# Kernel tuning notes

Hardware: AMD Instinct MI355X
Metric: run time of the kernel (lower is better)

The kernel has to match this reference:

```python
import jax, jax.numpy as jnp
import numpy as np

E = 50000      # entity_total
R = 100        # relation_total
DIM = 128      # config.dim
M = 10         # max_context_num
M1 = M + 1
T = 2 * R + 2  # entity_gcn_weight rows (2R+1) + appended zero row
B = 1024


def setup_inputs() -> dict:
    key = jax.random.key(0)
    ks = jax.random.split(key, 40)
    f = jnp.float32
    stdv = 1.0 / np.sqrt(DIM)
    inp = {}
    inp['entity_emb'] = jax.random.normal(ks[0], (E, DIM), f) * 0.05
    inp['relation_emb'] = jax.random.normal(ks[1], (R, DIM), f) * 0.05
    ec = jax.random.normal(ks[2], (E + 1, DIM), f) * 0.05
    inp['entity_context'] = ec.at[E].set(0.0)   # padding_idx row = 0
    rc = jax.random.normal(ks[3], (R + 1, DIM), f) * 0.05
    inp['relation_context'] = rc.at[R].set(0.0)
    inp['entity_gcn_weight'] = jax.random.uniform(ks[4], (2 * R + 1, DIM, DIM), f, -stdv, stdv)
    inp['relation_gcn_weight'] = jax.random.uniform(ks[5], (DIM, DIM), f, -stdv, stdv)
    inp['gate_entity'] = jax.random.uniform(ks[6], (DIM,), f)
    inp['gate_relation'] = jax.random.uniform(ks[7], (DIM,), f)
    inp['v_ent'] = jax.random.uniform(ks[8], (DIM,), f)
    inp['v_rel'] = jax.random.uniform(ks[9], (DIM,), f)
    inp['pos_h'] = jax.random.randint(ks[10], (B,), 0, E)
    inp['pos_r'] = jax.random.randint(ks[11], (B,), 0, R)
    inp['pos_t'] = jax.random.randint(ks[12], (B,), 0, E)
    inp['neg_h'] = jax.random.randint(ks[13], (B,), 0, E)
    inp['neg_r'] = jax.random.randint(ks[14], (B,), 0, R)
    inp['neg_t'] = jax.random.randint(ks[15], (B,), 0, E)
    inp['ph_adj'] = jax.random.randint(ks[16], (B, M), 0, E + 1)
    inp['pt_adj'] = jax.random.randint(ks[17], (B, M), 0, E + 1)
    inp['nh_adj'] = jax.random.randint(ks[18], (B, M), 0, E + 1)
    inp['nt_adj'] = jax.random.randint(ks[19], (B, M), 0, E + 1)
    inp['pr_adj'] = jax.random.randint(ks[20], (B, M, 2), 0, R + 1)
    inp['nr_adj'] = jax.random.randint(ks[21], (B, M, 2), 0, R + 1)
    inp['ph_R'] = jax.random.randint(ks[22], (B, M1, M1), 0, T)
    inp['pt_R'] = jax.random.randint(ks[23], (B, M1, M1), 0, T)
    inp['nh_R'] = jax.random.randint(ks[24], (B, M1, M1), 0, T)
    inp['nt_R'] = jax.random.randint(ks[25], (B, M1, M1), 0, T)
    inp['ph_nn'] = jax.random.randint(ks[26], (B,), 0, M)
    inp['pt_nn'] = jax.random.randint(ks[27], (B,), 0, M)
    inp['nh_nn'] = jax.random.randint(ks[28], (B,), 0, M)
    inp['nt_nn'] = jax.random.randint(ks[29], (B,), 0, M)
    inp['ph_D'] = jax.random.uniform(ks[30], (B, M1, M1), f)
    inp['pt_D'] = jax.random.uniform(ks[31], (B, M1, M1), f)
    inp['nh_D'] = jax.random.uniform(ks[32], (B, M1, M1), f)
    inp['nt_D'] = jax.random.uniform(ks[33], (B, M1, M1), f)
    inp['pr_A'] = jax.random.normal(ks[34], (B, M1, M1), f)
    inp['nr_A'] = jax.random.normal(ks[35], (B, M1, M1), f)
    return inp


def reference(entity_emb, relation_emb, entity_context, relation_context,
              entity_gcn_weight, relation_gcn_weight, gate_entity, gate_relation,
              v_ent, v_rel,
              pos_h, pos_r, pos_t, neg_h, neg_r, neg_t,
              ph_adj, pt_adj, nh_adj, nt_adj, pr_adj, nr_adj,
              ph_R, pt_R, nh_R, nt_R, ph_nn, pt_nn, nh_nn, nt_nn,
              ph_D, pt_D, nh_D, nt_D, pr_A, nr_A):
    # weight table with trailing zero row (padding relation type T-1)
    Wfull = jnp.concatenate(
        [entity_gcn_weight, jnp.zeros((1, DIM, DIM), entity_gcn_weight.dtype)], axis=0)

    def ent_ctx(vec, adj_idx):
        # center vector + M gathered context vectors -> [B, M1, d]
        return jnp.concatenate([vec[:, None, :], entity_context[adj_idx]], axis=1)

    def rel_ctx(vec, adj_idx):
        # relation context comes in (head,tail) pairs, summed over the 2
        a = relation_context[adj_idx].sum(axis=2)  # [B, M, d]
        return jnp.concatenate([vec[:, None, :], a], axis=1)

    def rgcn(Rt, Dm, nn_, H):
        # vectorized R-GCN: out[b,j] = relu(sum_k D[b,j,k] * H[b,j] @ W[Rt[b,j,k]])
        # restricted to the dynamic (n+1)x(n+1) block via masking.
        j = jnp.arange(M1)
        valid = j[None, :] <= nn_[:, None]                 # [B, M1]
        pair = valid[:, :, None] & valid[:, None, :]       # [B, M1, M1]
        Rm = jnp.where(pair, Rt, T - 1)                    # pad -> zero weight
        Dd = jnp.where(pair, Dm, jnp.zeros((), Dm.dtype))
        # segment-reduce D over relation types: C[b,j,t] = sum_{k: Rm=t} D[b,j,k]
        C = (jax.nn.one_hot(Rm, T, dtype=H.dtype) * Dd[..., None]).sum(axis=2)  # [B,M1,T]
        S = jnp.einsum('bjt,tde->bjde', C, Wfull)          # [B, M1, d, d]
        out = jax.nn.relu(jnp.einsum('bjd,bjde->bje', H, S))
        return jnp.where(valid[..., None], out, jnp.zeros((), out.dtype))

    def gcn_rel(A, H):
        return jax.nn.relu(jnp.einsum('bij,bjd,de->bie', A, H, relation_gcn_weight))

    def subgraph(o, adj, v):
        # attention over context rows, then weighted sum
        tmp = jax.nn.relu(adj * o[:, None, :])             # [B, M1, d]
        alpha = jax.nn.softmax(tmp @ v, axis=1)            # [B, M1]
        return jnp.sum(alpha[..., None] * adj, axis=1)     # [B, d]

    p_h = entity_emb[pos_h]; p_t = entity_emb[pos_t]; p_r = relation_emb[pos_r]
    n_h = entity_emb[neg_h]; n_t = entity_emb[neg_t]; n_r = relation_emb[neg_r]

    ph_v = rgcn(ph_R, ph_D, ph_nn, ent_ctx(p_h, ph_adj))
    pt_v = rgcn(pt_R, pt_D, pt_nn, ent_ctx(p_t, pt_adj))
    nh_v = rgcn(nh_R, nh_D, nh_nn, ent_ctx(n_h, nh_adj))
    nt_v = rgcn(nt_R, nt_D, nt_nn, ent_ctx(n_t, nt_adj))
    pr_v = gcn_rel(pr_A, rel_ctx(p_r, pr_adj))
    nr_v = gcn_rel(nr_A, rel_ctx(n_r, nr_adj))

    ph_sg = subgraph(p_h, ph_v, v_ent); pt_sg = subgraph(p_t, pt_v, v_ent)
    nh_sg = subgraph(n_h, nh_v, v_ent); nt_sg = subgraph(n_t, nt_v, v_ent)
    pr_sg = subgraph(p_r, pr_v, v_rel); nr_sg = subgraph(n_r, nr_v, v_rel)

    ge = jax.nn.sigmoid(gate_entity)
    gr = jax.nn.sigmoid(gate_relation)
    ph_o = ge * p_h + (1 - ge) * ph_sg
    pt_o = ge * p_t + (1 - ge) * pt_sg
    nh_o = ge * n_h + (1 - ge) * nh_sg
    nt_o = ge * n_t + (1 - ge) * nt_sg
    pr_o = gr * p_r + (1 - gr) * pr_sg
    nr_o = gr * n_r + (1 - gr) * nr_sg

    p_score = jnp.linalg.norm(ph_o + pr_o - pt_o, ord=2, axis=1)
    n_score = jnp.linalg.norm(nh_o + nr_o - nt_o, ord=2, axis=1)
    return (p_score, n_score)
```

## Files before the change

### kernel.cpp

```cpp
#include <hip/hip_runtime.h>
#include <math.h>

#define B_   1024
#define M_   10
#define M1_  11
#define DIM_ 128
#define NW_  201
#define NQUAD_ (4*B_*M1_*M1_)
#define IPB_  64
#define SLOTS_ 2048
#define NSPLIT_ 16
#define SCATB_ 121
#define WTILES_ ((NW_+1)*16)

typedef __attribute__((ext_vector_type(8))) short bf16x8;
typedef __attribute__((ext_vector_type(4))) float f32x4;

struct GatherPtrs {
    const int* center[4];
    const int* adj[4];
    const int* nn[4];
    const int* Rt[4];
    const float* Dm[4];
};

struct RelPtrs {
    const int* center[2];
    const int* adj2[2];
    const float* A[2];
};

__device__ __forceinline__ unsigned short f2bf(float f) {
    union { float f; unsigned u; } v; v.f = f;
    const unsigned r = v.u + 0x7FFFu + ((v.u >> 16) & 1u);
    return (unsigned short)(r >> 16);
}

template <int N>
__device__ __forceinline__ void block_reduce_bcast(float (&p)[N], float (*sred)[N],
                                                   int e, float (&sc)[N])
{
    #pragma unroll
    for (int off = 32; off; off >>= 1)
        #pragma unroll
        for (int i = 0; i < N; ++i) p[i] += __shfl_xor(p[i], off, 64);
    __syncthreads();
    if ((e & 63) == 0) {
        #pragma unroll
        for (int i = 0; i < N; ++i) sred[e >> 6][i] = p[i];
    }
    __syncthreads();
    #pragma unroll
    for (int i = 0; i < N; ++i) sc[i] = sred[0][i] + sred[1][i];
}

__device__ __forceinline__ float attn_pool(const float (&vm)[M1_], float o, float ve,
                                           float (*sred)[M1_], int e)
{
    float p[M1_];
    #pragma unroll
    for (int j = 0; j < M1_; ++j) p[j] = fmaxf(vm[j] * o, 0.f) * ve;
    float sc[M1_];
    block_reduce_bcast<M1_>(p, sred, e, sc);
    float mx = sc[0];
    #pragma unroll
    for (int j = 1; j < M1_; ++j) mx = fmaxf(mx, sc[j]);
    float s = 0.f, ex[M1_];
    #pragma unroll
    for (int j = 0; j < M1_; ++j) { ex[j] = expf(sc[j] - mx); s += ex[j]; }
    const float inv = 1.f / s;
    float sg = 0.f;
    #pragma unroll
    for (int j = 0; j < M1_; ++j) sg += ex[j] * inv * vm[j];
    return sg;
}

__global__ __launch_bounds__(256)
void wconv_kernel(const float* __restrict__ W, const float* __restrict__ Wr,
                  unsigned short* __restrict__ WT)
{
    __shared__ float tile[32][33];
    const int tl = blockIdx.x;
    const int t = tl >> 4, sub = tl & 15;
    const int bd = (sub >> 2) * 32, be = (sub & 3) * 32;
    const float* Ws = (t < NW_) ? (W + (size_t)t * DIM_ * DIM_) : Wr;
    unsigned short* Wd = WT + (size_t)t * DIM_ * DIM_;
    const int tx = threadIdx.x & 31, ty = threadIdx.x >> 5;
    #pragma unroll
    for (int r = 0; r < 32; r += 8)
        tile[r + ty][tx] = Ws[(bd + r + ty) * DIM_ + be + tx];
    __syncthreads();
    #pragma unroll
    for (int r = 0; r < 32; r += 8)
        Wd[(be + r + ty) * DIM_ + bd + tx] = f2bf(tile[tx][r + ty]);
}

__global__ __launch_bounds__(1024)
void scatter_kernel(GatherPtrs gp, int* __restrict__ cursor,
                    int* __restrict__ items)
{
    __shared__ int lh[NW_];
    __shared__ int lbase[NW_];
    const int tid = threadIdx.x;
    if (tid < NW_) lh[tid] = 0;
    __syncthreads();
    int rr[4], rk[4], pk[4];
    #pragma unroll
    for (int s = 0; s < 4; ++s) {
        const int idx = blockIdx.x * 4096 + s * 1024 + tid;
        const int c = idx / (B_ * M1_ * M1_);
        const int rem = idx % (B_ * M1_ * M1_);
        const int b = rem / (M1_ * M1_);
        const int jk = rem % (M1_ * M1_);
        const int j = jk / M1_, k = jk % M1_;
        const int n = gp.nn[c][b];
        rr[s] = -1;
        if (j <= n && k <= n) {
            const int r = gp.Rt[c][rem];
            if (r < NW_) {
                rr[s] = r;
                rk[s] = atomicAdd(&lh[r], 1);
                pk[s] = (c << 18) | (b << 8) | (j << 4) | k;
            }
        }
    }
    __syncthreads();
    if (tid < NW_) lbase[tid] = lh[tid] ? atomicAdd(&cursor[tid], lh[tid]) : 0;
    __syncthreads();
    #pragma unroll
    for (int s = 0; s < 4; ++s)
        if (rr[s] >= 0) {
            const int slot = lbase[rr[s]] + rk[s];
            if (slot < SLOTS_) items[rr[s] * SLOTS_ + slot] = pk[s];
        }
}

template <bool FAST>
__global__ __launch_bounds__(256)
void rgcn_gemm(GatherPtrs gp,
               const float* __restrict__ ent_emb,
               const float* __restrict__ ent_ctx,
               const unsigned short* __restrict__ WT,
               const int* __restrict__ items,
               const int* __restrict__ cursor,
               _Float16* __restrict__ partial,
               float* __restrict__ vent)
{
    __shared__ unsigned short sH[IPB_ * DIM_];
    __shared__ int sQ[IPB_];

    const int t = blockIdx.y, s = blockIdx.x;
    const int cnt = min(cursor[t], SLOTS_);
    const int nch = (cnt + IPB_ - 1) >> 6;
    if (s >= nch) return;
    const int tid = threadIdx.x;
    const int* ibase = items + t * SLOTS_;
    const unsigned short* Wp = WT + (size_t)t * DIM_ * DIM_;
    const int w = tid >> 6, l = tid & 63;
    const int lr = l & 15, lk = l >> 4;

    for (int ch = s; ch < nch; ch += NSPLIT_) {
        const int istart = ch * IPB_;
        const int nItems = min(IPB_, cnt - istart);

        {
            int p4[4];
            #pragma unroll
            for (int it4 = 0; it4 < 4; ++it4) {
                const int it = (it4 * 256 + tid) >> 4;
                p4[it4] = (it < nItems) ? ibase[istart + it] : -1;
            }
            const float* srow[4];
            float dsc[4];
            #pragma unroll
            for (int it4 = 0; it4 < 4; ++it4) {
                const int m = it4 * 256 + tid;
                const int it = m >> 4, chd = m & 15;
                const int p = p4[it4];
                if (p >= 0) {
                    const int c = p >> 18, b = (p >> 8) & 1023, j = (p >> 4) & 15, k = p & 15;
                    if (chd == 0) sQ[it] = ((c * B_ + b) * M1_ + j) * M1_ + k;
                    srow[it4] = (j == 0)
                        ? ent_emb + (size_t)gp.center[c][b] * DIM_
                        : ent_ctx + (size_t)gp.adj[c][b * M_ + (j - 1)] * DIM_;
                    dsc[it4] = gp.Dm[c][(b * M1_ + j) * M1_ + k];
                } else {
                    if (chd == 0) sQ[it] = -1;
                    srow[it4] = nullptr;
                }
            }
            float4 va[4], vb[4];
            #pragma unroll
            for (int it4 = 0; it4 < 4; ++it4) {
                const int chd = (it4 * 256 + tid) & 15;
                if (srow[it4]) {
                    const float4* s4 = (const float4*)srow[it4] + chd * 2;
                    va[it4] = s4[0]; vb[it4] = s4[1];
                }
            }
            #pragma unroll
            for (int it4 = 0; it4 < 4; ++it4) {
                const int m = it4 * 256 + tid;
                const int it = m >> 4, chd = m & 15;
                uint4 pkd;
                if (srow[it4]) {
                    const float d = dsc[it4];
                    pkd.x = (unsigned)f2bf(va[it4].x * d) | ((unsigned)f2bf(va[it4].y * d) << 16);
                    pkd.y = (unsigned)f2bf(va[it4].z * d) | ((unsigned)f2bf(va[it4].w * d) << 16);
                    pkd.z = (unsigned)f2bf(vb[it4].x * d) | ((unsigned)f2bf(vb[it4].y * d) << 16);
                    pkd.w = (unsigned)f2bf(vb[it4].z * d) | ((unsigned)f2bf(vb[it4].w * d) << 16);
                } else {
                    pkd.x = pkd.y = pkd.z = pkd.w = 0u;
                }
                const int o = chd * 16;
                const int so = it * 256 + (o ^ ((it & 7) << 4));
                *reinterpret_cast<uint4*>(reinterpret_cast<char*>(sH) + so) = pkd;
            }
        }
        __syncthreads();

        const f32x4 z = {0.f, 0.f, 0.f, 0.f};
        f32x4 acc[4][2];
        #pragma unroll
        for (int mi = 0; mi < 4; ++mi) { acc[mi][0] = z; acc[mi][1] = z; }

        #pragma unroll
        for (int kb = 0; kb < 4; ++kb) {
            const int o = kb * 64 + lk * 16;
            bf16x8 af[4], bfr[2];
            #pragma unroll
            for (int ni = 0; ni < 2; ++ni) {
                const int row = (2 * w + ni) * 16 + lr;
                bfr[ni] = *reinterpret_cast<const bf16x8*>(Wp + (size_t)row * DIM_ + kb * 32 + lk * 8);
            }
            #pragma unroll
            for (int mi = 0; mi < 4; ++mi) {
                const int row = mi * 16 + lr;
                af[mi] = *reinterpret_cast<const bf16x8*>(
                    reinterpret_cast<const char*>(sH) + row * 256 + (o ^ ((row & 7) << 4)));
            }
            #pragma unroll
            for (int mi = 0; mi < 4; ++mi)
                #pragma unroll
                for (int ni = 0; ni < 2; ++ni)
                    acc[mi][ni] = __builtin_amdgcn_mfma_f32_16x16x32_bf16(
                        af[mi], bfr[ni], acc[mi][ni], 0, 0, 0);
        }

        #pragma unroll
        for (int mi = 0; mi < 4; ++mi) {
            #pragma unroll
            for (int j = 0; j < 4; ++j) {
                const int it = mi * 16 + lk * 4 + j;
                const int q = sQ[it];
                if (q >= 0) {
                    #pragma unroll
                    for (int ni = 0; ni < 2; ++ni) {
                        const int col = (2 * w + ni) * 16 + lr;
                        if (FAST) {
                            partial[(size_t)q * DIM_ + col] = (_Float16)acc[mi][ni][j];
                        } else {
                            unsafeAtomicAdd(vent + (size_t)(q / M1_) * DIM_ + col,
                                            acc[mi][ni][j]);
                        }
                    }
                }
            }
        }
        __syncthreads();
    }
}

template <bool FAST>
__global__ __launch_bounds__(128)
void pool_kernel(GatherPtrs gp, RelPtrs rp,
                 const float* __restrict__ ent_emb,
                 const float* __restrict__ rel_emb,
                 const float* __restrict__ rel_ctx,
                 const unsigned short* __restrict__ WT,
                 const float* __restrict__ v_ent,
                 const float* __restrict__ v_rel,
                 const _Float16* __restrict__ partial,
                 const float* __restrict__ vent,
                 float* __restrict__ sgbuf)
{
    __shared__ float sred[2][M1_];
    const int b = blockIdx.x, c = blockIdx.y, e = threadIdx.x;

    if (c < 4) {
        __shared__ int sRt[M1_ * M1_];
        const int n = gp.nn[c][b];
        if (FAST && e < M1_ * M1_) sRt[e] = gp.Rt[c][b * (M1_ * M1_) + e];
        __syncthreads();

        const float o = ent_emb[(size_t)gp.center[c][b] * DIM_ + e];
        float vm[M1_];
        if (FAST) {
            #pragma unroll
            for (int j = 0; j < M1_; ++j) {
                float s = 0.f;
                if (j <= n) {
                    const int base = (c * B_ + b) * (M1_ * M1_) + j * M1_;
                    #pragma unroll
                    for (int k = 0; k < M1_; ++k) {
                        const float v = (float)partial[(size_t)(base + k) * DIM_ + e];
                        s += (k <= n && sRt[j * M1_ + k] < NW_) ? v : 0.f;
                    }
                    s = fmaxf(s, 0.f);
                }
                vm[j] = s;
            }
        } else {
            const float* vmat = vent + ((size_t)(c * B_ + b)) * M1_ * DIM_;
            #pragma unroll
            for (int j = 0; j < M1_; ++j)
                vm[j] = (j <= n) ? fmaxf(vmat[j * DIM_ + e], 0.f) : 0.f;
        }
        const float sg = attn_pool(vm, o, v_ent[e], sred, e);
        sgbuf[((size_t)c * B_ + b) * DIM_ + e] = sg;
    } else {
        __shared__ float sA[M1_ * M1_];
        __shared__ unsigned short sAH[16 * DIM_];
        __shared__ float sOut[M1_][DIM_];
        const int cse = c - 4;
        const int* adj2 = rp.adj2[cse];

        float h[M1_];
        const float o = rel_emb[(size_t)rp.center[cse][b] * DIM_ + e];
        h[0] = o;
        #pragma unroll
        for (int j = 1; j < M1_; ++j) {
            const int a0 = adj2[((b * M_) + (j - 1)) * 2 + 0];
            const int a1 = adj2[((b * M_) + (j - 1)) * 2 + 1];
            h[j] = rel_ctx[(size_t)a0 * DIM_ + e] + rel_ctx[(size_t)a1 * DIM_ + e];
        }
        if (e < M1_ * M1_) sA[e] = rp.A[cse][b * (M1_ * M1_) + e];
        __syncthreads();

        #pragma unroll
        for (int i = 0; i < M1_; ++i) {
            float s = 0.f;
            #pragma unroll
            for (int jj = 0; jj < M1_; ++jj) s += sA[i * M1_ + jj] * h[jj];
            *reinterpret_cast<unsigned short*>(
                reinterpret_cast<char*>(sAH) + i * 256 + ((2 * e) ^ ((i & 7) << 4))) = f2bf(s);
        }
        #pragma unroll
        for (int i = M1_; i < 16; ++i)
            *reinterpret_cast<unsigned short*>(
                reinterpret_cast<char*>(sAH) + i * 256 + ((2 * e) ^ ((i & 7) << 4))) = 0;
        __syncthreads();

        const int w = e >> 6, l = e & 63;
        const int lr = l & 15, lk = l >> 4;
        const unsigned short* WrT = WT + (size_t)NW_ * DIM_ * DIM_;
        const f32x4 z = {0.f, 0.f, 0.f, 0.f};
        f32x4 acc[4] = {z, z, z, z};
        #pragma unroll
        for (int kb = 0; kb < 4; ++kb) {
            const bf16x8 af = *reinterpret_cast<const bf16x8*>(
                reinterpret_cast<const char*>(sAH) + lr * 256 + ((kb * 64 + lk * 16) ^ ((lr & 7) << 4)));
            #pragma unroll
            for (int ni = 0; ni < 4; ++ni) {
                const int cb = w * 4 + ni;
                const bf16x8 bfr = *reinterpret_cast<const bf16x8*>(
                    WrT + (size_t)(cb * 16 + lr) * DIM_ + kb * 32 + lk * 8);
                acc[ni] = __builtin_amdgcn_mfma_f32_16x16x32_bf16(af, bfr, acc[ni], 0, 0, 0);
            }
        }
        #pragma unroll
        for (int ni = 0; ni < 4; ++ni) {
            const int col = (w * 4 + ni) * 16 + lr;
            #pragma unroll
            for (int j = 0; j < 4; ++j) {
                const int i = lk * 4 + j;
                if (i < M1_) sOut[i][col] = fmaxf(acc[ni][j], 0.f);
            }
        }
        __syncthreads();

        float vm[M1_];
        #pragma unroll
        for (int i = 0; i < M1_; ++i) vm[i] = sOut[i][e];
        const float sg = attn_pool(vm, o, v_rel[e], sred, e);
        sgbuf[((size_t)c * B_ + b) * DIM_ + e] = sg;
    }
}

__global__ __launch_bounds__(128)
void score_kernel(GatherPtrs gp,
                  const float* __restrict__ ent_emb,
                  const float* __restrict__ rel_emb,
                  const int* __restrict__ pos_r, const int* __restrict__ neg_r,
                  const float* __restrict__ gate_e, const float* __restrict__ gate_r,
                  const float* __restrict__ sgbuf,
                  float* __restrict__ out)
{
    __shared__ float sred[2][2];
    const int b = blockIdx.x, e = threadIdx.x;

    float cvec[4], osg[4];
    #pragma unroll
    for (int c = 0; c < 4; ++c) {
        cvec[c] = ent_emb[(size_t)gp.center[c][b] * DIM_ + e];
        osg[c] = sgbuf[((size_t)c * B_ + b) * DIM_ + e];
    }
    const float rvec0 = rel_emb[(size_t)pos_r[b] * DIM_ + e];
    const float rvec1 = rel_emb[(size_t)neg_r[b] * DIM_ + e];
    const float rsg0 = sgbuf[((size_t)4 * B_ + b) * DIM_ + e];
    const float rsg1 = sgbuf[((size_t)5 * B_ + b) * DIM_ + e];

    const float ge = 1.f / (1.f + expf(-gate_e[e]));
    const float gr = 1.f / (1.f + expf(-gate_r[e]));
    const float ph_o = ge * cvec[0] + (1.f - ge) * osg[0];
    const float pt_o = ge * cvec[1] + (1.f - ge) * osg[1];
    const float nh_o = ge * cvec[2] + (1.f - ge) * osg[2];
    const float nt_o = ge * cvec[3] + (1.f - ge) * osg[3];
    const float pr_o = gr * rvec0 + (1.f - gr) * rsg0;
    const float nr_o = gr * rvec1 + (1.f - gr) * rsg1;

    const float pv = ph_o + pr_o - pt_o;
    const float nv = nh_o + nr_o - nt_o;
    float p2[2] = { pv * pv, nv * nv };
    float sc2[2];
    block_reduce_bcast<2>(p2, sred, e, sc2);
    if (e == 0) { out[b] = sqrtf(sc2[0]); out[B_ + b] = sqrtf(sc2[1]); }
}

extern "C" void kernel_launch(void* const* d_in, const int* in_sizes, int n_in,
                              void* d_out, int out_size, void* d_ws, size_t ws_size,
                              hipStream_t stream)
{
    const float* entity_emb   = (const float*)d_in[0];
    const float* relation_emb = (const float*)d_in[1];
    const float* entity_ctx   = (const float*)d_in[2];
    const float* relation_ctx = (const float*)d_in[3];
    const float* egw          = (const float*)d_in[4];
    const float* rgw          = (const float*)d_in[5];
    const float* gate_e       = (const float*)d_in[6];
    const float* gate_r       = (const float*)d_in[7];
    const float* v_ent        = (const float*)d_in[8];
    const float* v_rel        = (const float*)d_in[9];
    const int* pos_h = (const int*)d_in[10];
    const int* pos_r = (const int*)d_in[11];
    const int* pos_t = (const int*)d_in[12];
    const int* neg_h = (const int*)d_in[13];
    const int* neg_r = (const int*)d_in[14];
    const int* neg_t = (const int*)d_in[15];
    const int* ph_adj = (const int*)d_in[16];
    const int* pt_adj = (const int*)d_in[17];
    const int* nh_adj = (const int*)d_in[18];
    const int* nt_adj = (const int*)d_in[19];
    const int* pr_adj = (const int*)d_in[20];
    const int* nr_adj = (const int*)d_in[21];
    const int* ph_R = (const int*)d_in[22];
    const int* pt_R = (const int*)d_in[23];
    const int* nh_R = (const int*)d_in[24];
    const int* nt_R = (const int*)d_in[25];
    const int* ph_nn = (const int*)d_in[26];
    const int* pt_nn = (const int*)d_in[27];
    const int* nh_nn = (const int*)d_in[28];
    const int* nt_nn = (const int*)d_in[29];
    const float* ph_D = (const float*)d_in[30];
    const float* pt_D = (const float*)d_in[31];
    const float* nh_D = (const float*)d_in[32];
    const float* nt_D = (const float*)d_in[33];
    const float* pr_A = (const float*)d_in[34];
    const float* nr_A = (const float*)d_in[35];

    GatherPtrs gp;
    gp.center[0] = pos_h; gp.center[1] = pos_t; gp.center[2] = neg_h; gp.center[3] = neg_t;
    gp.adj[0] = ph_adj; gp.adj[1] = pt_adj; gp.adj[2] = nh_adj; gp.adj[3] = nt_adj;
    gp.nn[0] = ph_nn; gp.nn[1] = pt_nn; gp.nn[2] = nh_nn; gp.nn[3] = nt_nn;
    gp.Rt[0] = ph_R; gp.Rt[1] = pt_R; gp.Rt[2] = nh_R; gp.Rt[3] = nt_R;
    gp.Dm[0] = ph_D; gp.Dm[1] = pt_D; gp.Dm[2] = nh_D; gp.Dm[3] = nt_D;

    RelPtrs rp;
    rp.center[0] = pos_r; rp.center[1] = neg_r;
    rp.adj2[0] = pr_adj; rp.adj2[1] = nr_adj;
    rp.A[0] = pr_A; rp.A[1] = nr_A;

    char* wsb = (char*)d_ws;
    const size_t partialBytes = (size_t)NQUAD_ * DIM_ * 2;
    const size_t itemsBytes   = (size_t)NW_ * SLOTS_ * 4;
    const size_t metaBytes    = 4096;
    const size_t wtBytes      = (size_t)(NW_ + 1) * DIM_ * DIM_ * 2;
    const size_t sgBytes      = (size_t)6 * B_ * DIM_ * 4;
    const size_t fastNeed = partialBytes + itemsBytes + metaBytes + wtBytes;
    const bool fast = (ws_size >= fastNeed);

    if (fast) {
        _Float16* partial = (_Float16*)wsb;
        int* items  = (int*)(wsb + partialBytes);
        int* cursor = (int*)(wsb + partialBytes + itemsBytes);
        char* wsg = wsb + partialBytes + itemsBytes + metaBytes;
        unsigned short* WT = (unsigned short*)wsg;
        float* sgbuf       = (float*)wsg;

        hipMemsetAsync(cursor, 0, 1024, stream);
        wconv_kernel<<<dim3(WTILES_), dim3(256), 0, stream>>>(egw, rgw, WT);
        scatter_kernel<<<dim3(SCATB_), dim3(1024), 0, stream>>>(gp, cursor, items);
        rgcn_gemm<true><<<dim3(NSPLIT_, NW_), dim3(256), 0, stream>>>(
            gp, entity_emb, entity_ctx, WT, items, cursor, partial, nullptr);
        pool_kernel<true><<<dim3(B_, 6), dim3(128), 0, stream>>>(
            gp, rp, entity_emb, relation_emb, relation_ctx, WT,
            v_ent, v_rel, partial, nullptr, sgbuf);
        score_kernel<<<dim3(B_), dim3(128), 0, stream>>>(
            gp, entity_emb, relation_emb, pos_r, neg_r, gate_e, gate_r, sgbuf, (float*)d_out);
    } else {
        float* vent = (float*)wsb;
        const size_t ventBytes = (size_t)4 * B_ * M1_ * DIM_ * 4;
        unsigned short* WT = (unsigned short*)(wsb + ventBytes);
        float* sgbuf = (float*)(wsb + ventBytes + wtBytes);
        int* items   = (int*)(wsb + ventBytes + wtBytes + sgBytes);
        int* cursor  = (int*)(wsb + ventBytes + wtBytes + sgBytes + itemsBytes);

        hipMemsetAsync(vent, 0, ventBytes, stream);
        hipMemsetAsync(cursor, 0, 1024, stream);
        wconv_kernel<<<dim3(WTILES_), dim3(256), 0, stream>>>(egw, rgw, WT);
        scatter_kernel<<<dim3(SCATB_), dim3(1024), 0, stream>>>(gp, cursor, items);
        rgcn_gemm<false><<<dim3(NSPLIT_, NW_), dim3(256), 0, stream>>>(
            gp, entity_emb, entity_ctx, WT, items, cursor, nullptr, vent);
        pool_kernel<false><<<dim3(B_, 6), dim3(128), 0, stream>>>(
            gp, rp, entity_emb, relation_emb, relation_ctx, WT,
            v_ent, v_rel, nullptr, vent, sgbuf);
        score_kernel<<<dim3(B_), dim3(128), 0, stream>>>(
            gp, entity_emb, relation_emb, pos_r, neg_r, gate_e, gate_r, sgbuf, (float*)d_out);
    }
}
```

Measured before the change: 109.9 us.

## Fuse prep kernels, pre-gather bf16 rows, and flatten GEMM grid per chunk

Merges the weight transpose/convert and relation-bucket scatter kernels into one prep launch. When the workspace is large enough, that launch also gathers every entity/context row once into a bf16 buffer, so the GEMM loads contiguous bf16 rows instead of re-gathering fp32 rows per item. The D scaling moves from the input staging to the GEMM epilogue. The GEMM grid becomes one block per 64-item chunk (32 per relation) instead of a strided split loop. This trades one fewer launch and less redundant gather traffic for an extra write and read of the gathered row buffer, plus more, mostly idle, blocks.

```diff
diff --git a/kernel.cpp b/kernel.cpp
--- a/kernel.cpp
+++ b/kernel.cpp
@@ -9,9 +9,11 @@
 #define NQUAD_ (4*B_*M1_*M1_)
 #define IPB_  64
 #define SLOTS_ 2048
-#define NSPLIT_ 16
 #define SCATB_ 121
 #define WTILES_ ((NW_+1)*16)
+#define HROWS_ (4*B_*M1_)
+#define HROWB_ (HROWS_/16)
+#define GEMMB_ (NW_*32)
 
 typedef __attribute__((ext_vector_type(8))) short bf16x8;
 typedef __attribute__((ext_vector_type(4))) float f32x4;
@@ -76,71 +78,93 @@
 }
 
 __global__ __launch_bounds__(256)
-void wconv_kernel(const float* __restrict__ W, const float* __restrict__ Wr,
-                  unsigned short* __restrict__ WT)
-{
-    __shared__ float tile[32][33];
-    const int tl = blockIdx.x;
-    const int t = tl >> 4, sub = tl & 15;
-    const int bd = (sub >> 2) * 32, be = (sub & 3) * 32;
-    const float* Ws = (t < NW_) ? (W + (size_t)t * DIM_ * DIM_) : Wr;
-    unsigned short* Wd = WT + (size_t)t * DIM_ * DIM_;
-    const int tx = threadIdx.x & 31, ty = threadIdx.x >> 5;
-    #pragma unroll
-    for (int r = 0; r < 32; r += 8)
-        tile[r + ty][tx] = Ws[(bd + r + ty) * DIM_ + be + tx];
-    __syncthreads();
-    #pragma unroll
-    for (int r = 0; r < 32; r += 8)
-        Wd[(be + r + ty) * DIM_ + bd + tx] = f2bf(tile[tx][r + ty]);
-}
-
-__global__ __launch_bounds__(1024)
-void scatter_kernel(GatherPtrs gp, int* __restrict__ cursor,
-                    int* __restrict__ items)
+void prep_kernel(GatherPtrs gp,
+                 const float* __restrict__ W, const float* __restrict__ Wr,
+                 const float* __restrict__ ent_emb,
+                 const float* __restrict__ ent_ctx,
+                 unsigned short* __restrict__ WT,
+                 unsigned short* __restrict__ Hd,
+                 int* __restrict__ cursor, int* __restrict__ items)
 {
     __shared__ int lh[NW_];
     __shared__ int lbase[NW_];
+    __shared__ float tile[32][33];
     const int tid = threadIdx.x;
-    if (tid < NW_) lh[tid] = 0;
-    __syncthreads();
-    int rr[4], rk[4], pk[4];
-    #pragma unroll
-    for (int s = 0; s < 4; ++s) {
-        const int idx = blockIdx.x * 4096 + s * 1024 + tid;
-        const int c = idx / (B_ * M1_ * M1_);
-        const int rem = idx % (B_ * M1_ * M1_);
-        const int b = rem / (M1_ * M1_);
-        const int jk = rem % (M1_ * M1_);
-        const int j = jk / M1_, k = jk % M1_;
-        const int n = gp.nn[c][b];
-        rr[s] = -1;
-        if (j <= n && k <= n) {
-            const int r = gp.Rt[c][rem];
-            if (r < NW_) {
-                rr[s] = r;
-                rk[s] = atomicAdd(&lh[r], 1);
-                pk[s] = (c << 18) | (b << 8) | (j << 4) | k;
-            }
-        }
-    }
-    __syncthreads();
-    if (tid < NW_) lbase[tid] = lh[tid] ? atomicAdd(&cursor[tid], lh[tid]) : 0;
-    __syncthreads();
-    #pragma unroll
-    for (int s = 0; s < 4; ++s)
-        if (rr[s] >= 0) {
-            const int slot = lbase[rr[s]] + rk[s];
-            if (slot < SLOTS_) items[rr[s] * SLOTS_ + slot] = pk[s];
-        }
-}
-
-template <bool FAST>
+    const int bid = blockIdx.x;
+
+    if (bid < SCATB_) {
+        if (tid < NW_) lh[tid] = 0;
+        __syncthreads();
+        int rr[16], rk[16], pk[16];
+        #pragma unroll
+        for (int s = 0; s < 16; ++s) {
+            const int idx = bid * 4096 + s * 256 + tid;
+            const int c = idx / (B_ * M1_ * M1_);
+            const int rem = idx % (B_ * M1_ * M1_);
+            const int b = rem / (M1_ * M1_);
+            const int jk = rem % (M1_ * M1_);
+            const int j = jk / M1_, k = jk % M1_;
+            const int n = gp.nn[c][b];
+            rr[s] = -1;
+            if (j <= n && k <= n) {
+                const int r = gp.Rt[c][rem];
+                if (r < NW_) {
+                    rr[s] = r;
+                    rk[s] = atomicAdd(&lh[r], 1);
+                    pk[s] = (c << 18) | (b << 8) | (j << 4) | k;
+                }
+            }
+        }
+        __syncthreads();
+        if (tid < NW_) lbase[tid] = lh[tid] ? atomicAdd(&cursor[tid], lh[tid]) : 0;
+        __syncthreads();
+        #pragma unroll
+        for (int s = 0; s < 16; ++s)
+            if (rr[s] >= 0) {
+                const int slot = lbase[rr[s]] + rk[s];
+                if (slot < SLOTS_) items[rr[s] * SLOTS_ + slot] = pk[s];
+            }
+    } else if (bid < SCATB_ + WTILES_) {
+        const int tl = bid - SCATB_;
+        const int t = tl >> 4, sub = tl & 15;
+        const int bd = (sub >> 2) * 32, be = (sub & 3) * 32;
+        const float* Ws = (t < NW_) ? (W + (size_t)t * DIM_ * DIM_) : Wr;
+        unsigned short* Wd = WT + (size_t)t * DIM_ * DIM_;
+        const int tx = tid & 31, ty = tid >> 5;
+        #pragma unroll
+        for (int r = 0; r < 32; r += 8)
+            tile[r + ty][tx] = Ws[(bd + r + ty) * DIM_ + be + tx];
+        __syncthreads();
+        #pragma unroll
+        for (int r = 0; r < 32; r += 8)
+            Wd[(be + r + ty) * DIM_ + bd + tx] = f2bf(tile[tx][r + ty]);
+    } else {
+        const int rid = (bid - SCATB_ - WTILES_) * 16 + (tid >> 4);
+        const int part = tid & 15;
+        const int c = rid / (B_ * M1_);
+        const int rem = rid % (B_ * M1_);
+        const int b = rem / M1_, j = rem % M1_;
+        const float* srow = (j == 0)
+            ? ent_emb + (size_t)gp.center[c][b] * DIM_
+            : ent_ctx + (size_t)gp.adj[c][b * M_ + (j - 1)] * DIM_;
+        const float4* s4 = (const float4*)srow + part * 2;
+        const float4 v0 = s4[0], v1 = s4[1];
+        uint4 pkd;
+        pkd.x = (unsigned)f2bf(v0.x) | ((unsigned)f2bf(v0.y) << 16);
+        pkd.y = (unsigned)f2bf(v0.z) | ((unsigned)f2bf(v0.w) << 16);
+        pkd.z = (unsigned)f2bf(v1.x) | ((unsigned)f2bf(v1.y) << 16);
+        pkd.w = (unsigned)f2bf(v1.z) | ((unsigned)f2bf(v1.w) << 16);
+        *reinterpret_cast<uint4*>(Hd + (size_t)rid * DIM_ + part * 8) = pkd;
+    }
+}
+
+template <int MODE>
 __global__ __launch_bounds__(256)
 void rgcn_gemm(GatherPtrs gp,
                const float* __restrict__ ent_emb,
                const float* __restrict__ ent_ctx,
                const unsigned short* __restrict__ WT,
+               const unsigned short* __restrict__ Hd,
                const int* __restrict__ items,
                const int* __restrict__ cursor,
                _Float16* __restrict__ partial,
@@ -148,126 +172,103 @@
 {
     __shared__ unsigned short sH[IPB_ * DIM_];
     __shared__ int sQ[IPB_];
-
-    const int t = blockIdx.y, s = blockIdx.x;
+    __shared__ float sD[IPB_];
+
+    const int bid = blockIdx.x;
+    const int t = bid >> 5, ch = bid & 31;
     const int cnt = min(cursor[t], SLOTS_);
-    const int nch = (cnt + IPB_ - 1) >> 6;
-    if (s >= nch) return;
+    if (ch * IPB_ >= cnt) return;
+    const int istart = ch * IPB_;
+    const int nItems = min(IPB_, cnt - istart);
     const int tid = threadIdx.x;
     const int* ibase = items + t * SLOTS_;
-    const unsigned short* Wp = WT + (size_t)t * DIM_ * DIM_;
+
+    #pragma unroll
+    for (int it4 = 0; it4 < 4; ++it4) {
+        const int m = it4 * 256 + tid;
+        const int it = m >> 4, chd = m & 15;
+        uint4 pkd;
+        if (it < nItems) {
+            const int p = ibase[istart + it];
+            const int c = p >> 18, b = (p >> 8) & 1023, j = (p >> 4) & 15, k = p & 15;
+            const int row = (c * B_ + b) * M1_ + j;
+            if (chd == 0) {
+                sQ[it] = row * M1_ + k;
+                sD[it] = gp.Dm[c][(b * M1_ + j) * M1_ + k];
+            }
+            if (MODE == 1) {
+                pkd = *reinterpret_cast<const uint4*>(Hd + (size_t)row * DIM_ + chd * 8);
+            } else {
+                const float* srow = (j == 0)
+                    ? ent_emb + (size_t)gp.center[c][b] * DIM_
+                    : ent_ctx + (size_t)gp.adj[c][b * M_ + (j - 1)] * DIM_;
+                const float4* s4 = (const float4*)srow + chd * 2;
+                const float4 v0 = s4[0], v1 = s4[1];
+                pkd.x = (unsigned)f2bf(v0.x) | ((unsigned)f2bf(v0.y) << 16);
+                pkd.y = (unsigned)f2bf(v0.z) | ((unsigned)f2bf(v0.w) << 16);
+                pkd.z = (unsigned)f2bf(v1.x) | ((unsigned)f2bf(v1.y) << 16);
+                pkd.w = (unsigned)f2bf(v1.z) | ((unsigned)f2bf(v1.w) << 16);
+            }
+        } else {
+            if (chd == 0) { sQ[it] = -1; sD[it] = 0.f; }
+            pkd.x = pkd.y = pkd.z = pkd.w = 0u;
+        }
+        const int so = it * 256 + ((chd * 16) ^ ((it & 7) << 4));
+        *reinterpret_cast<uint4*>(reinterpret_cast<char*>(sH) + so) = pkd;
+    }
+    __syncthreads();
+
     const int w = tid >> 6, l = tid & 63;
     const int lr = l & 15, lk = l >> 4;
-
-    for (int ch = s; ch < nch; ch += NSPLIT_) {
-        const int istart = ch * IPB_;
-        const int nItems = min(IPB_, cnt - istart);
-
-        {
-            int p4[4];
+    const unsigned short* Wp = WT + (size_t)t * DIM_ * DIM_;
+    const f32x4 z = {0.f, 0.f, 0.f, 0.f};
+    f32x4 acc[4][2];
+    #pragma unroll
+    for (int mi = 0; mi < 4; ++mi) { acc[mi][0] = z; acc[mi][1] = z; }
+
+    #pragma unroll
+    for (int kb = 0; kb < 4; ++kb) {
+        const int o = kb * 64 + lk * 16;
+        bf16x8 af[4], bfr[2];
+        #pragma unroll
+        for (int ni = 0; ni < 2; ++ni) {
+            const int row = (2 * w + ni) * 16 + lr;
+            bfr[ni] = *reinterpret_cast<const bf16x8*>(Wp + (size_t)row * DIM_ + kb * 32 + lk * 8);
+        }
+        #pragma unroll
+        for (int mi = 0; mi < 4; ++mi) {
+            const int row = mi * 16 + lr;
+            af[mi] = *reinterpret_cast<const bf16x8*>(
+                reinterpret_cast<const char*>(sH) + row * 256 + (o ^ ((row & 7) << 4)));
+        }
+        #pragma unroll
+        for (int mi = 0; mi < 4; ++mi)
             #pragma unroll
-            for (int it4 = 0; it4 < 4; ++it4) {
-                const int it = (it4 * 256 + tid) >> 4;
-                p4[it4] = (it < nItems) ? ibase[istart + it] : -1;
-            }
-            const float* srow[4];
-            float dsc[4];
-            #pragma unroll
-            for (int it4 = 0; it4 < 4; ++it4) {
-                const int m = it4 * 256 + tid;
-                const int it = m >> 4, chd = m & 15;
-                const int p = p4[it4];
-                if (p >= 0) {
-                    const int c = p >> 18, b = (p >> 8) & 1023, j = (p >> 4) & 15, k = p & 15;
-                    if (chd == 0) sQ[it] = ((c * B_ + b) * M1_ + j) * M1_ + k;
-                    srow[it4] = (j == 0)
-                        ? ent_emb + (size_t)gp.center[c][b] * DIM_
-                        : ent_ctx + (size_t)gp.adj[c][b * M_ + (j - 1)] * DIM_;
-                    dsc[it4] = gp.Dm[c][(b * M1_ + j) * M1_ + k];
-                } else {
-                    if (chd == 0) sQ[it] = -1;
-                    srow[it4] = nullptr;
-                }
-            }
-            float4 va[4], vb[4];
-            #pragma unroll
-            for (int it4 = 0; it4 < 4; ++it4) {
-                const int chd = (it4 * 256 + tid) & 15;
-                if (srow[it4]) {
-                    const float4* s4 = (const float4*)srow[it4] + chd * 2;
-                    va[it4] = s4[0]; vb[it4] = s4[1];
-                }
-            }
-            #pragma unroll
-            for (int it4 = 0; it4 < 4; ++it4) {
-                const int m = it4 * 256 + tid;
-                const int it = m >> 4, chd = m & 15;
-                uint4 pkd;
-                if (srow[it4]) {
-                    const float d = dsc[it4];
-                    pkd.x = (unsigned)f2bf(va[it4].x * d) | ((unsigned)f2bf(va[it4].y * d) << 16);
-                    pkd.y = (unsigned)f2bf(va[it4].z * d) | ((unsigned)f2bf(va[it4].w * d) << 16);
-                    pkd.z = (unsigned)f2bf(vb[it4].x * d) | ((unsigned)f2bf(vb[it4].y * d) << 16);
-                    pkd.w = (unsigned)f2bf(vb[it4].z * d) | ((unsigned)f2bf(vb[it4].w * d) << 16);
-                } else {
-                    pkd.x = pkd.y = pkd.z = pkd.w = 0u;
-                }
-                const int o = chd * 16;
-                const int so = it * 256 + (o ^ ((it & 7) << 4));
-                *reinterpret_cast<uint4*>(reinterpret_cast<char*>(sH) + so) = pkd;
-            }
-        }
-        __syncthreads();
-
-        const f32x4 z = {0.f, 0.f, 0.f, 0.f};
-        f32x4 acc[4][2];
-        #pragma unroll
-        for (int mi = 0; mi < 4; ++mi) { acc[mi][0] = z; acc[mi][1] = z; }
-
-        #pragma unroll
-        for (int kb = 0; kb < 4; ++kb) {
-            const int o = kb * 64 + lk * 16;
-            bf16x8 af[4], bfr[2];
-            #pragma unroll
-            for (int ni = 0; ni < 2; ++ni) {
-                const int row = (2 * w + ni) * 16 + lr;
-                bfr[ni] = *reinterpret_cast<const bf16x8*>(Wp + (size_t)row * DIM_ + kb * 32 + lk * 8);
-            }
-            #pragma unroll
-            for (int mi = 0; mi < 4; ++mi) {
-                const int row = mi * 16 + lr;
-                af[mi] = *reinterpret_cast<const bf16x8*>(
-                    reinterpret_cast<const char*>(sH) + row * 256 + (o ^ ((row & 7) << 4)));
-            }
-            #pragma unroll
-            for (int mi = 0; mi < 4; ++mi)
+            for (int ni = 0; ni < 2; ++ni)
+                acc[mi][ni] = __builtin_amdgcn_mfma_f32_16x16x32_bf16(
+                    af[mi], bfr[ni], acc[mi][ni], 0, 0, 0);
+    }
+
+    #pragma unroll
+    for (int mi = 0; mi < 4; ++mi) {
+        #pragma unroll
+        for (int jj = 0; jj < 4; ++jj) {
+            const int it = mi * 16 + lk * 4 + jj;
+            const int q = sQ[it];
+            if (q >= 0) {
+                const float d = sD[it];
                 #pragma unroll
-                for (int ni = 0; ni < 2; ++ni)
-                    acc[mi][ni] = __builtin_amdgcn_mfma_f32_16x16x32_bf16(
-                        af[mi], bfr[ni], acc[mi][ni], 0, 0, 0);
-        }
-
-        #pragma unroll
-        for (int mi = 0; mi < 4; ++mi) {
-            #pragma unroll
-            for (int j = 0; j < 4; ++j) {
-                const int it = mi * 16 + lk * 4 + j;
-                const int q = sQ[it];
-                if (q >= 0) {
-                    #pragma unroll
-                    for (int ni = 0; ni < 2; ++ni) {
-                        const int col = (2 * w + ni) * 16 + lr;
-                        if (FAST) {
-                            partial[(size_t)q * DIM_ + col] = (_Float16)acc[mi][ni][j];
-                        } else {
-                            unsafeAtomicAdd(vent + (size_t)(q / M1_) * DIM_ + col,
-                                            acc[mi][ni][j]);
-                        }
+                for (int ni = 0; ni < 2; ++ni) {
+                    const int col = (2 * w + ni) * 16 + lr;
+                    const float val = acc[mi][ni][jj] * d;
+                    if (MODE <= 1) {
+                        partial[(size_t)q * DIM_ + col] = (_Float16)val;
+                    } else {
+                        unsafeAtomicAdd(vent + (size_t)(q / M1_) * DIM_ + col, val);
                     }
                 }
             }
         }
-        __syncthreads();
     }
 }
 
@@ -372,9 +373,9 @@
         for (int ni = 0; ni < 4; ++ni) {
             const int col = (w * 4 + ni) * 16 + lr;
             #pragma unroll
-            for (int j = 0; j < 4; ++j) {
-                const int i = lk * 4 + j;
-                if (i < M1_) sOut[i][col] = fmaxf(acc[ni][j], 0.f);
+            for (int jj = 0; jj < 4; ++jj) {
+                const int i = lk * 4 + jj;
+                if (i < M1_) sOut[i][col] = fmaxf(acc[ni][jj], 0.f);
             }
         }
         __syncthreads();
@@ -485,23 +486,32 @@
     const size_t itemsBytes   = (size_t)NW_ * SLOTS_ * 4;
     const size_t metaBytes    = 4096;
     const size_t wtBytes      = (size_t)(NW_ + 1) * DIM_ * DIM_ * 2;
+    const size_t hdBytes      = (size_t)HROWS_ * DIM_ * 2;
     const size_t sgBytes      = (size_t)6 * B_ * DIM_ * 4;
-    const size_t fastNeed = partialBytes + itemsBytes + metaBytes + wtBytes;
-    const bool fast = (ws_size >= fastNeed);
-
-    if (fast) {
+    const size_t needB = partialBytes + itemsBytes + metaBytes + wtBytes;
+    const size_t needA = needB + hdBytes;
+    const int tier = (ws_size >= needA) ? 0 : (ws_size >= needB) ? 1 : 2;
+
+    if (tier <= 1) {
         _Float16* partial = (_Float16*)wsb;
         int* items  = (int*)(wsb + partialBytes);
         int* cursor = (int*)(wsb + partialBytes + itemsBytes);
         char* wsg = wsb + partialBytes + itemsBytes + metaBytes;
         unsigned short* WT = (unsigned short*)wsg;
         float* sgbuf       = (float*)wsg;
+        unsigned short* Hd = (tier == 0) ? (unsigned short*)(wsg + wtBytes) : nullptr;
 
         hipMemsetAsync(cursor, 0, 1024, stream);
-        wconv_kernel<<<dim3(WTILES_), dim3(256), 0, stream>>>(egw, rgw, WT);
-        scatter_kernel<<<dim3(SCATB_), dim3(1024), 0, stream>>>(gp, cursor, items);
-        rgcn_gemm<true><<<dim3(NSPLIT_, NW_), dim3(256), 0, stream>>>(
-            gp, entity_emb, entity_ctx, WT, items, cursor, partial, nullptr);
+        const int prepb = SCATB_ + WTILES_ + ((tier == 0) ? HROWB_ : 0);
+        prep_kernel<<<dim3(prepb), dim3(256), 0, stream>>>(
+            gp, egw, rgw, entity_emb, entity_ctx, WT, Hd, cursor, items);
+        if (tier == 0) {
+            rgcn_gemm<1><<<dim3(GEMMB_), dim3(256), 0, stream>>>(
+                gp, entity_emb, entity_ctx, WT, Hd, items, cursor, partial, nullptr);
+        } else {
+            rgcn_gemm<0><<<dim3(GEMMB_), dim3(256), 0, stream>>>(
+                gp, entity_emb, entity_ctx, WT, nullptr, items, cursor, partial, nullptr);
+        }
         pool_kernel<true><<<dim3(B_, 6), dim3(128), 0, stream>>>(
             gp, rp, entity_emb, relation_emb, relation_ctx, WT,
             v_ent, v_rel, partial, nullptr, sgbuf);
@@ -517,10 +527,10 @@
 
         hipMemsetAsync(vent, 0, ventBytes, stream);
         hipMemsetAsync(cursor, 0, 1024, stream);
-        wconv_kernel<<<dim3(WTILES_), dim3(256), 0, stream>>>(egw, rgw, WT);
-        scatter_kernel<<<dim3(SCATB_), dim3(1024), 0, stream>>>(gp, cursor, items);
-        rgcn_gemm<false><<<dim3(NSPLIT_, NW_), dim3(256), 0, stream>>>(
-            gp, entity_emb, entity_ctx, WT, items, cursor, nullptr, vent);
+        prep_kernel<<<dim3(SCATB_ + WTILES_), dim3(256), 0, stream>>>(
+            gp, egw, rgw, entity_emb, entity_ctx, WT, nullptr, cursor, items);
+        rgcn_gemm<2><<<dim3(GEMMB_), dim3(256), 0, stream>>>(
+            gp, entity_emb, entity_ctx, WT, nullptr, items, cursor, nullptr, vent);
         pool_kernel<false><<<dim3(B_, 6), dim3(128), 0, stream>>>(
             gp, rp, entity_emb, relation_emb, relation_ctx, WT,
             v_ent, v_rel, nullptr, vent, sgbuf);
```

New measurement: 119.1 us. +8.3%, slower.
